# Performance work log

Measured on AMD Instinct MI355X. Metric: run time of the kernel, lower is better.

Reference implementation:

```python
import jax, jax.numpy as jnp
import numpy as np

T, IN, OUT, GS, L, R = 64, 4096, 12288, 128, 4, 16
G = IN // GS  # 32 groups along in_features


def setup_inputs() -> dict:
    key = jax.random.key(0)
    ks = jax.random.split(key, 7)
    x = jax.random.normal(ks[0], (T, IN), dtype=jnp.float32)
    qweight = jax.random.randint(ks[1], (OUT, IN), 0, 16, dtype=jnp.int32)      # int4 codes 0..15
    zeros = jax.random.randint(ks[2], (OUT, G), 0, 16, dtype=jnp.int32)         # per-group zero points
    scales = jax.random.uniform(ks[3], (OUT, G), dtype=jnp.float32) * 0.02      # per-group scales
    up = jax.random.normal(ks[4], (L, OUT, R), dtype=jnp.float32) * 0.02        # LoRA up weights
    down = jax.random.normal(ks[5], (L, R, IN), dtype=jnp.float32) * 0.02       # LoRA down weights
    lora_scales = jax.random.uniform(ks[6], (L,), dtype=jnp.float32)            # scale*alpha/rank folded
    return dict(x=x, qweight=qweight, zeros=zeros, scales=scales, up=up, down=down, lora_scales=lora_scales)


def _dequant(qweight, zeros, scales):
    # AWQ group dequant: w = (q - zero) * scale, groups of GS along in_features
    q = qweight.reshape(OUT, G, GS).astype(jnp.float32)
    z = zeros.astype(jnp.float32)[:, :, None]
    w = (q - z) * scales[:, :, None]
    return w.reshape(OUT, IN)


def reference(x, qweight, zeros, scales, up, down, lora_scales):
    # base quantized linear: y = x @ dequant(W).T
    w = _dequant(qweight, zeros, scales)
    y = jnp.einsum('ti,oi->to', x, w)
    # all LoRA adapters applied in one batched pass (matches looped accumulate)
    t = jnp.einsum('ti,lri->tlr', x, down)               # [T, L, R]
    y = y + jnp.einsum('tlr,lor,l->to', t, up, lora_scales)
    return y
```

## Files before the change

kernel.cpp:

```cpp
#include <hip/hip_runtime.h>
#include <hip/hip_bf16.h>

#define T_DIM   64
#define IN_DIM  4096
#define OUT_DIM 12288
#define NGROUP  32
#define R_DIM   16
#define LR      64

#define BN 16
#define BK 128
#define NCHUNK (IN_DIM / BK)
#define W_STRIDE (BK + 8)
#define T_STRIDE (LR + 8)

#define KSPLIT 8
#define KSLICE (IN_DIM / KSPLIT)

#define PART_FLOATS (KSPLIT * T_DIM * LR)
#define XBF_BYTE_OFF (PART_FLOATS * 4)

typedef __bf16 bf16x4 __attribute__((ext_vector_type(4)));
typedef __bf16 bf16x8 __attribute__((ext_vector_type(8)));
typedef float  f32x4  __attribute__((ext_vector_type(4)));

__device__ __forceinline__ void barrier_lgkm() {
    asm volatile("" ::: "memory");
    __builtin_amdgcn_s_waitcnt(0xC07F);
    __builtin_amdgcn_s_barrier();
    asm volatile("" ::: "memory");
}

__global__ __launch_bounds__(256) void prep_kernel(
    const float* __restrict__ x, const float* __restrict__ down,
    const float* __restrict__ lora_scales, float* __restrict__ part,
    __bf16* __restrict__ xbf2)
{
    const int tid = threadIdx.x;
    const int bid = blockIdx.x;

    if (bid < 64) {
        const int rt = bid & 3;
        const int kb_base = (bid >> 2) * 8;
        const int lane = tid & 63, w = tid >> 6;
        const int row  = rt * 16 + (lane & 15);
        const int qd   = lane >> 4;
#pragma unroll
        for (int i = 0; i < 2; ++i) {
            int kb   = kb_base + i * 4 + w;
            int col0 = kb * 32 + qd * 8;
            float4 v0 = *(const float4*)(x + row * IN_DIM + col0);
            float4 v1 = *(const float4*)(x + row * IN_DIM + col0 + 4);
            bf16x8 b;
            b[0] = (__bf16)v0.x; b[1] = (__bf16)v0.y;
            b[2] = (__bf16)v0.z; b[3] = (__bf16)v0.w;
            b[4] = (__bf16)v1.x; b[5] = (__bf16)v1.y;
            b[6] = (__bf16)v1.z; b[7] = (__bf16)v1.w;
            *(bf16x8*)(xbf2 + ((rt * 128 + kb) * 64 + lane) * 8) = b;
        }
        return;
    }

    __shared__ float d_lds[KSLICE];
    const int p  = bid - 64;
    const int c  = p & 63;
    const int ks = p >> 6;
    const float* dsl = down + c * IN_DIM + ks * KSLICE;
    for (int j = tid; j < KSLICE / 4; j += 256)
        ((float4*)d_lds)[j] = ((const float4*)dsl)[j];
    __syncthreads();
    const float ls = lora_scales[c >> 4];
    const int wave = tid >> 6, lane = tid & 63;
    for (int t = wave * 2; t < T_DIM; t += 8) {
        const float4* xr0 = (const float4*)(x + t * IN_DIM + ks * KSLICE);
        const float4* xr1 = (const float4*)(x + (t + 1) * IN_DIM + ks * KSLICE);
        float sa = 0.f, sb = 0.f;
#pragma unroll
        for (int j = 0; j < 2; ++j) {
            float4 dv = ((const float4*)d_lds)[lane + j * 64];
            float4 xa = xr0[lane + j * 64];
            float4 xb = xr1[lane + j * 64];
            sa += xa.x * dv.x + xa.y * dv.y + xa.z * dv.z + xa.w * dv.w;
            sb += xb.x * dv.x + xb.y * dv.y + xb.z * dv.z + xb.w * dv.w;
        }
        for (int off = 32; off; off >>= 1) {
            sa += __shfl_down(sa, off);
            sb += __shfl_down(sb, off);
        }
        if (lane == 0) {
            part[(ks * T_DIM + t) * LR + c]     = sa * ls;
            part[(ks * T_DIM + t + 1) * LR + c] = sb * ls;
        }
    }
}

__global__ __launch_bounds__(256, 3) void awq_lora_gemm_kernel(
    const __bf16* __restrict__ xbf2, const int* __restrict__ qweight,
    const int* __restrict__ zeros, const float* __restrict__ scales,
    const float* __restrict__ up, const float* __restrict__ part,
    float* __restrict__ out)
{
    __shared__ __bf16 w_lds[2][BN][W_STRIDE];
    __shared__ __bf16 t_lds[T_DIM][T_STRIDE];
    __shared__ float  s_lds[BN][NGROUP];
    __shared__ float  zs_lds[BN][NGROUP];

    const int tid  = threadIdx.x;
    const int n0   = blockIdx.x * BN;
    const int wave = tid >> 6, lane = tid & 63;
    const int lrow = lane & 15, quad = lane >> 4;

    int qrow[2], qcol[2], qoff[2];
#pragma unroll
    for (int it = 0; it < 2; ++it) {
        int e = (it * 256 + tid) * 4;
        qrow[it] = e >> 7; qcol[it] = e & 127;
        qoff[it] = (n0 + qrow[it]) * IN_DIM + qcol[it];
    }

    const __bf16* abase = xbf2 + wave * 65536 + lane * 8;

#pragma unroll
    for (int it = 0; it < 2; ++it) {
        int idx = it * 256 + tid;
        int row = idx >> 5, g = idx & 31;
        float s = scales[(n0 + row) * NGROUP + g];
        float z = (float)zeros[(n0 + row) * NGROUP + g];
        s_lds[row][g]  = s;
        zs_lds[row][g] = -z * s;
    }

    int4   qr0[2], qr1[2];
    bf16x8 ar0[4], ar1[4];
#pragma unroll
    for (int it = 0; it < 2; ++it) qr0[it] = *(const int4*)(qweight + qoff[it]);
#pragma unroll
    for (int kk = 0; kk < 4; ++kk) ar0[kk] = *(const bf16x8*)(abase + kk * 512);
#pragma unroll
    for (int it = 0; it < 2; ++it) qr1[it] = *(const int4*)(qweight + qoff[it] + BK);
#pragma unroll
    for (int kk = 0; kk < 4; ++kk) ar1[kk] = *(const bf16x8*)(abase + 2048 + kk * 512);

    f32x4 acc = {0.f, 0.f, 0.f, 0.f};

    barrier_lgkm();

    for (int ch = 0; ch < NCHUNK; ch += 2) {
#pragma unroll
        for (int it = 0; it < 2; ++it) {
            float s  = s_lds[qrow[it]][ch];
            float zs = zs_lds[qrow[it]][ch];
            bf16x4 w;
            w[0] = (__bf16)((float)qr0[it].x * s + zs);
            w[1] = (__bf16)((float)qr0[it].y * s + zs);
            w[2] = (__bf16)((float)qr0[it].z * s + zs);
            w[3] = (__bf16)((float)qr0[it].w * s + zs);
            *(bf16x4*)&w_lds[0][qrow[it]][qcol[it]] = w;
        }
        if (ch + 2 < NCHUNK) {
            const int k0 = (ch + 2) * BK;
#pragma unroll
            for (int it = 0; it < 2; ++it) qr0[it] = *(const int4*)(qweight + qoff[it] + k0);
        }
        barrier_lgkm();
#pragma unroll
        for (int kk = 0; kk < 4; ++kk) {
            const int ko = kk * 32 + quad * 8;
            bf16x8 b0 = *(const bf16x8*)&w_lds[0][lrow][ko];
            acc = __builtin_amdgcn_mfma_f32_16x16x32_bf16(ar0[kk], b0, acc, 0, 0, 0);
        }
        if (ch + 2 < NCHUNK) {
#pragma unroll
            for (int kk = 0; kk < 4; ++kk) ar0[kk] = *(const bf16x8*)(abase + (ch + 2) * 2048 + kk * 512);
        }

#pragma unroll
        for (int it = 0; it < 2; ++it) {
            float s  = s_lds[qrow[it]][ch + 1];
            float zs = zs_lds[qrow[it]][ch + 1];
            bf16x4 w;
            w[0] = (__bf16)((float)qr1[it].x * s + zs);
            w[1] = (__bf16)((float)qr1[it].y * s + zs);
            w[2] = (__bf16)((float)qr1[it].z * s + zs);
            w[3] = (__bf16)((float)qr1[it].w * s + zs);
            *(bf16x4*)&w_lds[1][qrow[it]][qcol[it]] = w;
        }
        if (ch + 3 < NCHUNK) {
            const int k0 = (ch + 3) * BK;
#pragma unroll
            for (int it = 0; it < 2; ++it) qr1[it] = *(const int4*)(qweight + qoff[it] + k0);
        }
        barrier_lgkm();
#pragma unroll
        for (int kk = 0; kk < 4; ++kk) {
            const int ko = kk * 32 + quad * 8;
            bf16x8 b0 = *(const bf16x8*)&w_lds[1][lrow][ko];
            acc = __builtin_amdgcn_mfma_f32_16x16x32_bf16(ar1[kk], b0, acc, 0, 0, 0);
        }
        if (ch + 3 < NCHUNK) {
#pragma unroll
            for (int kk = 0; kk < 4; ++kk) ar1[kk] = *(const bf16x8*)(abase + (ch + 3) * 2048 + kk * 512);
        }
    }

    {
        const f32x4* p4 = (const f32x4*)part;
#pragma unroll
        for (int it = 0; it < 4; ++it) {
            int u = it * 256 + tid;
            f32x4 s = p4[u];
#pragma unroll
            for (int p = 1; p < KSPLIT; ++p) s += p4[p * 1024 + u];
            bf16x4 bv;
            bv[0] = (__bf16)s[0]; bv[1] = (__bf16)s[1];
            bv[2] = (__bf16)s[2]; bv[3] = (__bf16)s[3];
            *(bf16x4*)&t_lds[u >> 4][(u & 15) * 4] = bv;
        }
    }
#pragma unroll
    for (int it = 0; it < 4; ++it) {
        int idx = it * 256 + tid;
        int oo = idx >> 6, cc = idx & 63;
        int l = cc >> 4, r = cc & 15;
        w_lds[0][oo][cc] = (__bf16)up[(l * OUT_DIM + n0 + oo) * R_DIM + r];
    }
    barrier_lgkm();
#pragma unroll
    for (int kk = 0; kk < 2; ++kk) {
        const int ko = kk * 32 + quad * 8;
        bf16x8 a  = *(const bf16x8*)&t_lds[wave * 16 + lrow][ko];
        bf16x8 b0 = *(const bf16x8*)&w_lds[0][lrow][ko];
        acc = __builtin_amdgcn_mfma_f32_16x16x32_bf16(a, b0, acc, 0, 0, 0);
    }

    const int o = n0 + lrow;
#pragma unroll
    for (int i = 0; i < 4; ++i) {
        const int t = wave * 16 + quad * 4 + i;
        out[t * OUT_DIM + o] = acc[i];
    }
}

extern "C" void kernel_launch(void* const* d_in, const int* in_sizes, int n_in,
                              void* d_out, int out_size, void* d_ws, size_t ws_size,
                              hipStream_t stream) {
    const float* x           = (const float*)d_in[0];
    const int*   qweight     = (const int*)d_in[1];
    const int*   zeros       = (const int*)d_in[2];
    const float* scales      = (const float*)d_in[3];
    const float* up          = (const float*)d_in[4];
    const float* down        = (const float*)d_in[5];
    const float* lora_scales = (const float*)d_in[6];
    float*  out  = (float*)d_out;
    float*  part = (float*)d_ws;
    __bf16* xbf2 = (__bf16*)((char*)d_ws + XBF_BYTE_OFF);

    hipLaunchKernelGGL(prep_kernel, dim3(64 + 64 * KSPLIT), dim3(256), 0, stream,
                       x, down, lora_scales, part, xbf2);
    hipLaunchKernelGGL(awq_lora_gemm_kernel, dim3(OUT_DIM / BN), dim3(256), 0, stream,
                       xbf2, qweight, zeros, scales, up, part, out);
}
```

Measured before the change: 301.6 us.

## Widen dequant stages to 256 columns and split x conversion across more blocks

Each pipeline stage of the GEMM kernel now dequantizes 256 in-feature columns per weight row instead of 128. Each thread holds four int4 weight loads per stage, and the activation fragments are reloaded in even/odd halves. This halves the number of LDS barriers and keeps more global weight traffic in flight, aimed at hiding latency on the int32 weight stream. The prep kernel's bf16 conversion of x is spread over twice as many blocks, one chunk per wave. The cost is higher register and LDS use, which could lower occupancy under the 3-blocks-per-CU launch bound.

```diff
diff --git a/kernel.cpp b/kernel.cpp
--- a/kernel.cpp
+++ b/kernel.cpp
@@ -9,9 +9,9 @@
 #define LR      64
 
 #define BN 16
-#define BK 128
-#define NCHUNK (IN_DIM / BK)
-#define W_STRIDE (BK + 8)
+#define BK2 256
+#define NSTAGE (IN_DIM / BK2)
+#define W_STRIDE (BK2 + 8)
 #define T_STRIDE (LR + 8)
 
 #define KSPLIT 8
@@ -39,30 +39,25 @@
     const int tid = threadIdx.x;
     const int bid = blockIdx.x;
 
-    if (bid < 64) {
+    if (bid < 128) {
         const int rt = bid & 3;
-        const int kb_base = (bid >> 2) * 8;
-        const int lane = tid & 63, w = tid >> 6;
+        const int kb = (bid >> 2) * 4 + (tid >> 6);
+        const int lane = tid & 63;
         const int row  = rt * 16 + (lane & 15);
-        const int qd   = lane >> 4;
-#pragma unroll
-        for (int i = 0; i < 2; ++i) {
-            int kb   = kb_base + i * 4 + w;
-            int col0 = kb * 32 + qd * 8;
-            float4 v0 = *(const float4*)(x + row * IN_DIM + col0);
-            float4 v1 = *(const float4*)(x + row * IN_DIM + col0 + 4);
-            bf16x8 b;
-            b[0] = (__bf16)v0.x; b[1] = (__bf16)v0.y;
-            b[2] = (__bf16)v0.z; b[3] = (__bf16)v0.w;
-            b[4] = (__bf16)v1.x; b[5] = (__bf16)v1.y;
-            b[6] = (__bf16)v1.z; b[7] = (__bf16)v1.w;
-            *(bf16x8*)(xbf2 + ((rt * 128 + kb) * 64 + lane) * 8) = b;
-        }
+        const int col0 = kb * 32 + (lane >> 4) * 8;
+        float4 v0 = *(const float4*)(x + row * IN_DIM + col0);
+        float4 v1 = *(const float4*)(x + row * IN_DIM + col0 + 4);
+        bf16x8 b;
+        b[0] = (__bf16)v0.x; b[1] = (__bf16)v0.y;
+        b[2] = (__bf16)v0.z; b[3] = (__bf16)v0.w;
+        b[4] = (__bf16)v1.x; b[5] = (__bf16)v1.y;
+        b[6] = (__bf16)v1.z; b[7] = (__bf16)v1.w;
+        *(bf16x8*)(xbf2 + ((rt * 128 + kb) * 64 + lane) * 8) = b;
         return;
     }
 
     __shared__ float d_lds[KSLICE];
-    const int p  = bid - 64;
+    const int p  = bid - 128;
     const int c  = p & 63;
     const int ks = p >> 6;
     const float* dsl = down + c * IN_DIM + ks * KSLICE;
@@ -110,13 +105,14 @@
     const int wave = tid >> 6, lane = tid & 63;
     const int lrow = lane & 15, quad = lane >> 4;
 
-    int qrow[2], qcol[2], qoff[2];
-#pragma unroll
-    for (int it = 0; it < 2; ++it) {
+    int qrow[4], qcol[4], qoff[4];
+#pragma unroll
+    for (int it = 0; it < 4; ++it) {
         int e = (it * 256 + tid) * 4;
-        qrow[it] = e >> 7; qcol[it] = e & 127;
+        qrow[it] = e >> 8; qcol[it] = e & 255;
         qoff[it] = (n0 + qrow[it]) * IN_DIM + qcol[it];
     }
+    const int ghalf = qcol[0] >> 7;
 
     const __bf16* abase = xbf2 + wave * 65536 + lane * 8;
 
@@ -130,76 +126,98 @@
         zs_lds[row][g] = -z * s;
     }
 
-    int4   qr0[2], qr1[2];
-    bf16x8 ar0[4], ar1[4];
-#pragma unroll
-    for (int it = 0; it < 2; ++it) qr0[it] = *(const int4*)(qweight + qoff[it]);
-#pragma unroll
-    for (int kk = 0; kk < 4; ++kk) ar0[kk] = *(const bf16x8*)(abase + kk * 512);
-#pragma unroll
-    for (int it = 0; it < 2; ++it) qr1[it] = *(const int4*)(qweight + qoff[it] + BK);
-#pragma unroll
-    for (int kk = 0; kk < 4; ++kk) ar1[kk] = *(const bf16x8*)(abase + 2048 + kk * 512);
+    int4   qa[4], qb[4];
+    bf16x8 arE[4], arO[4];
+#pragma unroll
+    for (int it = 0; it < 4; ++it) qa[it] = *(const int4*)(qweight + qoff[it]);
+#pragma unroll
+    for (int kk = 0; kk < 4; ++kk) arE[kk] = *(const bf16x8*)(abase + kk * 512);
+#pragma unroll
+    for (int it = 0; it < 4; ++it) qb[it] = *(const int4*)(qweight + qoff[it] + BK2);
+#pragma unroll
+    for (int kk = 0; kk < 4; ++kk) arO[kk] = *(const bf16x8*)(abase + 2048 + kk * 512);
 
     f32x4 acc = {0.f, 0.f, 0.f, 0.f};
 
     barrier_lgkm();
 
-    for (int ch = 0; ch < NCHUNK; ch += 2) {
-#pragma unroll
-        for (int it = 0; it < 2; ++it) {
-            float s  = s_lds[qrow[it]][ch];
-            float zs = zs_lds[qrow[it]][ch];
-            bf16x4 w;
-            w[0] = (__bf16)((float)qr0[it].x * s + zs);
-            w[1] = (__bf16)((float)qr0[it].y * s + zs);
-            w[2] = (__bf16)((float)qr0[it].z * s + zs);
-            w[3] = (__bf16)((float)qr0[it].w * s + zs);
-            *(bf16x4*)&w_lds[0][qrow[it]][qcol[it]] = w;
-        }
-        if (ch + 2 < NCHUNK) {
-            const int k0 = (ch + 2) * BK;
-#pragma unroll
-            for (int it = 0; it < 2; ++it) qr0[it] = *(const int4*)(qweight + qoff[it] + k0);
+    for (int s = 0; s < NSTAGE; s += 2) {
+        {
+            const int g0 = s * 2 + ghalf;
+#pragma unroll
+            for (int it = 0; it < 4; ++it) {
+                const float sc = s_lds[qrow[it]][g0];
+                const float zs = zs_lds[qrow[it]][g0];
+                bf16x4 w;
+                w[0] = (__bf16)((float)qa[it].x * sc + zs);
+                w[1] = (__bf16)((float)qa[it].y * sc + zs);
+                w[2] = (__bf16)((float)qa[it].z * sc + zs);
+                w[3] = (__bf16)((float)qa[it].w * sc + zs);
+                *(bf16x4*)&w_lds[0][qrow[it]][qcol[it]] = w;
+            }
+        }
+        if (s + 2 < NSTAGE) {
+            const int k0 = (s + 2) * BK2;
+#pragma unroll
+            for (int it = 0; it < 4; ++it) qa[it] = *(const int4*)(qweight + qoff[it] + k0);
         }
         barrier_lgkm();
 #pragma unroll
         for (int kk = 0; kk < 4; ++kk) {
             const int ko = kk * 32 + quad * 8;
             bf16x8 b0 = *(const bf16x8*)&w_lds[0][lrow][ko];
-            acc = __builtin_amdgcn_mfma_f32_16x16x32_bf16(ar0[kk], b0, acc, 0, 0, 0);
-        }
-        if (ch + 2 < NCHUNK) {
-#pragma unroll
-            for (int kk = 0; kk < 4; ++kk) ar0[kk] = *(const bf16x8*)(abase + (ch + 2) * 2048 + kk * 512);
-        }
-
-#pragma unroll
-        for (int it = 0; it < 2; ++it) {
-            float s  = s_lds[qrow[it]][ch + 1];
-            float zs = zs_lds[qrow[it]][ch + 1];
-            bf16x4 w;
-            w[0] = (__bf16)((float)qr1[it].x * s + zs);
-            w[1] = (__bf16)((float)qr1[it].y * s + zs);
-            w[2] = (__bf16)((float)qr1[it].z * s + zs);
-            w[3] = (__bf16)((float)qr1[it].w * s + zs);
-            *(bf16x4*)&w_lds[1][qrow[it]][qcol[it]] = w;
-        }
-        if (ch + 3 < NCHUNK) {
-            const int k0 = (ch + 3) * BK;
-#pragma unroll
-            for (int it = 0; it < 2; ++it) qr1[it] = *(const int4*)(qweight + qoff[it] + k0);
+            acc = __builtin_amdgcn_mfma_f32_16x16x32_bf16(arE[kk], b0, acc, 0, 0, 0);
+        }
+#pragma unroll
+        for (int kk = 0; kk < 4; ++kk) arE[kk] = *(const bf16x8*)(abase + (2*s + 2) * 2048 + kk * 512);
+#pragma unroll
+        for (int kk = 0; kk < 4; ++kk) {
+            const int ko = 128 + kk * 32 + quad * 8;
+            bf16x8 b0 = *(const bf16x8*)&w_lds[0][lrow][ko];
+            acc = __builtin_amdgcn_mfma_f32_16x16x32_bf16(arO[kk], b0, acc, 0, 0, 0);
+        }
+#pragma unroll
+        for (int kk = 0; kk < 4; ++kk) arO[kk] = *(const bf16x8*)(abase + (2*s + 3) * 2048 + kk * 512);
+
+        {
+            const int g0 = s * 2 + 2 + ghalf;
+#pragma unroll
+            for (int it = 0; it < 4; ++it) {
+                const float sc = s_lds[qrow[it]][g0];
+                const float zs = zs_lds[qrow[it]][g0];
+                bf16x4 w;
+                w[0] = (__bf16)((float)qb[it].x * sc + zs);
+                w[1] = (__bf16)((float)qb[it].y * sc + zs);
+                w[2] = (__bf16)((float)qb[it].z * sc + zs);
+                w[3] = (__bf16)((float)qb[it].w * sc + zs);
+                *(bf16x4*)&w_lds[1][qrow[it]][qcol[it]] = w;
+            }
+        }
+        if (s + 3 < NSTAGE) {
+            const int k0 = (s + 3) * BK2;
+#pragma unroll
+            for (int it = 0; it < 4; ++it) qb[it] = *(const int4*)(qweight + qoff[it] + k0);
         }
         barrier_lgkm();
 #pragma unroll
         for (int kk = 0; kk < 4; ++kk) {
             const int ko = kk * 32 + quad * 8;
             bf16x8 b0 = *(const bf16x8*)&w_lds[1][lrow][ko];
-            acc = __builtin_amdgcn_mfma_f32_16x16x32_bf16(ar1[kk], b0, acc, 0, 0, 0);
-        }
-        if (ch + 3 < NCHUNK) {
-#pragma unroll
-            for (int kk = 0; kk < 4; ++kk) ar1[kk] = *(const bf16x8*)(abase + (ch + 3) * 2048 + kk * 512);
+            acc = __builtin_amdgcn_mfma_f32_16x16x32_bf16(arE[kk], b0, acc, 0, 0, 0);
+        }
+        if (s + 2 < NSTAGE) {
+#pragma unroll
+            for (int kk = 0; kk < 4; ++kk) arE[kk] = *(const bf16x8*)(abase + (2*s + 4) * 2048 + kk * 512);
+        }
+#pragma unroll
+        for (int kk = 0; kk < 4; ++kk) {
+            const int ko = 128 + kk * 32 + quad * 8;
+            bf16x8 b0 = *(const bf16x8*)&w_lds[1][lrow][ko];
+            acc = __builtin_amdgcn_mfma_f32_16x16x32_bf16(arO[kk], b0, acc, 0, 0, 0);
+        }
+        if (s + 2 < NSTAGE) {
+#pragma unroll
+            for (int kk = 0; kk < 4; ++kk) arO[kk] = *(const bf16x8*)(abase + (2*s + 5) * 2048 + kk * 512);
         }
     }
 
@@ -255,7 +273,7 @@
     float*  part = (float*)d_ws;
     __bf16* xbf2 = (__bf16*)((char*)d_ws + XBF_BYTE_OFF);
 
-    hipLaunchKernelGGL(prep_kernel, dim3(64 + 64 * KSPLIT), dim3(256), 0, stream,
+    hipLaunchKernelGGL(prep_kernel, dim3(128 + 64 * KSPLIT), dim3(256), 0, stream,
                        x, down, lora_scales, part, xbf2);
     hipLaunchKernelGGL(awq_lora_gemm_kernel, dim3(OUT_DIM / BN), dim3(256), 0, stream,
                        xbf2, qweight, zeros, scales, up, part, out);
```

Result: faster. 295.2 us (-2.1%).
